# Optimization experiments

Hardware: AMD Instinct MI355X
Metric: run time of the kernel (lower is better)

Reference implementation:

```python
import jax, jax.numpy as jnp
import numpy as np

N = 50000
E = 400000
C = 64
H = 6  # heads, hardcoded in the module
NEG_SLOPE = 0.2
EPS = 1e-8


def setup_inputs() -> dict:
    key = jax.random.key(0)
    ks = jax.random.split(key, 10)
    x = jax.random.normal(ks[0], (N, C), dtype=jnp.float32)
    ei = jax.random.randint(ks[1], (2, E), 0, N)
    loop = jnp.arange(N)
    # forward() first calls add_remaining_self_loops -> GCN consumes edges + self loops
    src = jnp.concatenate([ei[0], loop])
    dst = jnp.concatenate([ei[1], loop])
    # gen_subs: subindex = self loops (i->i) plus reversed edges (t->i) for edge (i,t)
    sub_src = jnp.concatenate([loop, ei[1]])
    sub_dst = jnp.concatenate([loop, ei[0]])

    def glorot(k, shape):
        stdv = np.sqrt(6.0 / (shape[-2] + shape[-1]))
        return jax.random.uniform(k, shape, jnp.float32, -stdv, stdv)

    W_gcn = glorot(ks[2], (C, C))           # gnn_intra_cluster (GCNConv)
    b_gcn = jnp.zeros((C,), jnp.float32)
    weight = glorot(ks[3], (C, H * C))      # self.weight
    attention = glorot(ks[4], (1, H, 2 * C))  # self.attention
    W1 = glorot(ks[5], (C, C))              # simiConv.lin1 (no bias)
    W2 = glorot(ks[6], (C, 1))              # simiConv.lin2
    b2 = jnp.zeros((1,), jnp.float32)
    return {"x": x, "W_gcn": W_gcn, "b_gcn": b_gcn, "weight": weight,
            "attention": attention, "W1": W1, "W2": W2, "b2": b2,
            "src": src, "dst": dst, "sub_src": sub_src, "sub_dst": sub_dst}


def _gcn(x, W, b, src, dst, n):
    # PyG GCNConv's gcn_norm appends its own self loops on top of the ones
    # already added by forward()'s add_remaining_self_loops.
    loop = jnp.arange(n)
    s = jnp.concatenate([src, loop])
    d = jnp.concatenate([dst, loop])
    deg = jax.ops.segment_sum(jnp.ones_like(s, dtype=x.dtype), d, num_segments=n)
    dinv = jax.lax.rsqrt(jnp.maximum(deg, 1.0e-12))
    norm = dinv[s] * dinv[d]                      # [E']
    h = x @ W                                     # [N, C]
    out = jax.ops.segment_sum(h[s] * norm[:, None], d, num_segments=n)
    return out + b


def reference(x, W_gcn, b_gcn, weight, attention, W1, W2, b2,
              src, dst, sub_src, sub_dst):
    n = x.shape[0]
    # intra-cluster GCN
    xpj = _gcn(x, W_gcn, b_gcn, src, dst, n)      # [N, C]
    # multi-head attention pooling over subindex
    h = (xpj @ weight).reshape(n, H, C)           # [N, H, C]
    hi = h[sub_src]                               # [Es, H, C] (x_i in message)
    hmax = jax.ops.segment_max(hi, sub_dst, num_segments=n)  # [N, H, C]
    att_i = attention[:, :, :C]                   # [1, H, C]
    att_j = attention[:, :, C:]
    alpha = (hi * att_i).sum(-1) + (hmax[sub_dst] * att_j).sum(-1)  # [Es, H]
    alpha = jnp.where(alpha >= 0, alpha, NEG_SLOPE * alpha)
    # segment softmax over destination nodes (dropout p=0)
    amax = jax.ops.segment_max(alpha, sub_dst, num_segments=n)
    e = jnp.exp(alpha - amax[sub_dst])
    denom = jax.ops.segment_sum(e, sub_dst, num_segments=n)
    alpha = e / denom[sub_dst]
    xa = jax.ops.segment_sum(hi * alpha[:, :, None], sub_dst, num_segments=n)
    xm = xa.mean(axis=1)                          # [N, C]
    # simiConv score: message = x_cluster_i * cos(x_i, x_j), aggr='add'
    a = xm @ W1                                   # [N, C]
    bsc = xm @ W2 + b2                            # [N, 1]
    ai = a[sub_dst]
    aj = a[sub_src]
    cos = (ai * aj).sum(-1) / (jnp.maximum(jnp.linalg.norm(ai, axis=-1), EPS)
                               * jnp.maximum(jnp.linalg.norm(aj, axis=-1), EPS))
    score = jax.ops.segment_sum(bsc[sub_dst, 0] * cos, sub_dst, num_segments=n)
    fitness = jax.nn.sigmoid(score)               # [N]
    return fitness
```

## Files before the change

### kernel.cpp

```cpp
#include <hip/hip_runtime.h>
#include <math.h>

#define TPB 256
#define NEG_SLOPE 0.2f
#define COS_EPS 1e-8f
#define NH 6
#define GSTRIDE 68
#define DCACHE 12
#define SALS 8

__device__ inline float wave_sum64(float v) {
  #pragma unroll
  for (int off = 32; off > 0; off >>= 1) v += __shfl_down(v, off);
  return __shfl(v, 0);
}
__device__ inline float wave_max64(float v) {
  #pragma unroll
  for (int off = 32; off > 0; off >>= 1) v = fmaxf(v, __shfl_down(v, off));
  return __shfl(v, 0);
}
__device__ inline unsigned short f2bf(float f) {
  unsigned u = __float_as_uint(f);
  unsigned r = (u + 0x7fffu + ((u >> 16) & 1u)) >> 16;
  return (unsigned short)r;
}
__device__ inline float bf2f(unsigned short b) {
  return __uint_as_float(((unsigned)b) << 16);
}
__device__ inline unsigned packbf(float lo, float hi) {
  return (unsigned)f2bf(lo) | ((unsigned)f2bf(hi) << 16);
}
__device__ inline float bflo(unsigned u) { return __uint_as_float(u << 16); }
__device__ inline float bfhi(unsigned u) { return __uint_as_float(u & 0xffff0000u); }

#define GS_LOOP(i, total) \
  for (long i = (long)blockIdx.x * blockDim.x + threadIdx.x; i < (total); \
       i += (long)gridDim.x * blockDim.x)

__global__ void k_cnt(const int* __restrict__ dst, const int* __restrict__ sdst,
                      int* __restrict__ gcnt, int* __restrict__ scnt,
                      long en, long sen) {
  long mx = en > sen ? en : sen;
  GS_LOOP(e, mx) {
    if (e < en)  atomicAdd(&gcnt[dst[e]], 1);
    if (e < sen) atomicAdd(&scnt[sdst[e]], 1);
  }
}

__global__ __launch_bounds__(1024)
void k_scanA(const int* __restrict__ gcnt, const int* __restrict__ scnt,
             int* __restrict__ bsum, float* __restrict__ dinv, int n, int nb) {
  const int b = blockIdx.x;
  const bool isS = b >= nb;
  const int tb = isS ? b - nb : b;
  const int* cnt = isS ? scnt : gcnt;
  const int t = threadIdx.x;
  const int i0 = tb * 2048 + 2 * t;
  int v0 = (i0 < n) ? cnt[i0] : 0;
  int v1 = (i0 + 1 < n) ? cnt[i0 + 1] : 0;
  if (!isS) {
    if (i0 < n)     dinv[i0]     = rsqrtf((float)v0 + 1.0f);
    if (i0 + 1 < n) dinv[i0 + 1] = rsqrtf((float)v1 + 1.0f);
  }
  __shared__ int red[16];
  int x = v0 + v1;
  #pragma unroll
  for (int o = 32; o > 0; o >>= 1) x += __shfl_down(x, o);
  const int lane = t & 63, wv = t >> 6;
  if (lane == 0) red[wv] = x;
  __syncthreads();
  if (t < 64) {
    int w = (t < 16) ? red[t] : 0;
    #pragma unroll
    for (int o = 32; o > 0; o >>= 1) w += __shfl_down(w, o);
    if (t == 0) bsum[b] = w;
  }
}

__global__ void k_scanB(int* __restrict__ bsum, int nb) {
  const int lane = threadIdx.x;
  if (nb <= 32) {
    int half = lane >> 5, idx = lane & 31;
    int base = half * nb;
    int v = (idx < nb) ? bsum[base + idx] : 0;
    int orig = v;
    #pragma unroll
    for (int d2 = 1; d2 < 32; d2 <<= 1) {
      int y = __shfl_up(v, d2, 32);
      if (idx >= d2) v += y;
    }
    if (idx < nb) bsum[base + idx] = v - orig;
  } else if (lane == 0) {
    int run = 0;
    for (int i = 0; i < nb; ++i) { int v = bsum[i]; bsum[i] = run; run += v; }
    run = 0;
    for (int i = 0; i < nb; ++i) { int v = bsum[nb + i]; bsum[nb + i] = run; run += v; }
  }
}

__global__ __launch_bounds__(1024)
void k_scanC(const int* __restrict__ gcnt, int* __restrict__ goff, int* __restrict__ gcur,
             const int* __restrict__ scnt, int* __restrict__ soff, int* __restrict__ scur,
             const int* __restrict__ bsum, int n, int nb) {
  const int b = blockIdx.x;
  const bool isS = b >= nb;
  const int tb = isS ? b - nb : b;
  const int* cnt = isS ? scnt : gcnt;
  int* off = isS ? soff : goff;
  int* cur = isS ? scur : gcur;
  const int t = threadIdx.x;
  const int i0 = tb * 2048 + 2 * t;
  int v0 = (i0 < n) ? cnt[i0] : 0;
  int v1 = (i0 + 1 < n) ? cnt[i0 + 1] : 0;
  int s2 = v0 + v1;
  const int lane = t & 63, wv = t >> 6;
  int x = s2;
  #pragma unroll
  for (int d2 = 1; d2 < 64; d2 <<= 1) {
    int y = __shfl_up(x, d2);
    if (lane >= d2) x += y;
  }
  __shared__ int wsum[16];
  if (lane == 63) wsum[wv] = x;
  __syncthreads();
  if (t < 64) {
    int w = (t < 16) ? wsum[t] : 0;
    #pragma unroll
    for (int d2 = 1; d2 < 16; d2 <<= 1) {
      int y = __shfl_up(w, d2);
      if ((int)t >= d2) w += y;
    }
    if (t < 16) wsum[t] = w;
  }
  __syncthreads();
  int ex = x - s2 + (wv ? wsum[wv - 1] : 0) + bsum[b];
  if (i0 < n)     { cur[i0] = ex;          off[i0 + 1] = ex + v0; }
  if (i0 + 1 < n) { cur[i0 + 1] = ex + v0; off[i0 + 2] = ex + v0 + v1; }
  if (i0 == 0) off[0] = 0;
}

__global__ void k_scatter(const int* __restrict__ src, const int* __restrict__ dst,
                          const int* __restrict__ ssrc, const int* __restrict__ sdst,
                          int* __restrict__ gcur, int* __restrict__ gcsr,
                          int* __restrict__ scur, int* __restrict__ scsr,
                          long en, long sen) {
  long mx = en > sen ? en : sen;
  GS_LOOP(e, mx) {
    if (e < en)  { int d = dst[e];  int p = atomicAdd(&gcur[d], 1); gcsr[p] = src[e]; }
    if (e < sen) { int d = sdst[e]; int p = atomicAdd(&scur[d], 1); scsr[p] = ssrc[e]; }
  }
}

template <int MODE>
__global__ __launch_bounds__(256)
void k_gemm64v3(const float* __restrict__ A, const float* __restrict__ W,
                float* __restrict__ out32, unsigned short* __restrict__ out16,
                const float* __restrict__ W2, const float* __restrict__ b2,
                float* __restrict__ bsc, int n, int Mtot) {
  __shared__ float At[64 * GSTRIDE];
  __shared__ float Wl[64 * GSTRIDE];
  const int t  = threadIdx.x;
  const int tx = t & 15;
  const int ty = t >> 4;
  const int col0 = blockIdx.y * 64;
  const long row0 = (long)blockIdx.x * 64;

  #pragma unroll
  for (int i = 0; i < 4; ++i) {
    int k = ty + 16 * i;
    float4 wv = *(const float4*)&W[(long)k * Mtot + col0 + 4 * tx];
    *(float4*)&Wl[k * GSTRIDE + 4 * tx] = wv;
  }
  #pragma unroll
  for (int i = 0; i < 4; ++i) {
    int r = ty + 16 * i;
    long gr = row0 + r; if (gr >= n) gr = n - 1;
    float4 av = *(const float4*)&A[gr * 64 + 4 * tx];
    At[(4 * tx + 0) * GSTRIDE + r] = av.x;
    At[(4 * tx + 1) * GSTRIDE + r] = av.y;
    At[(4 * tx + 2) * GSTRIDE + r] = av.z;
    At[(4 * tx + 3) * GSTRIDE + r] = av.w;
  }
  __syncthreads();

  const int c0 = 4 * tx;
  const int r0 = 4 * ty;
  float acc[4][4] = {};
  #pragma unroll
  for (int k = 0; k < 64; ++k) {
    float4 av = *(const float4*)&At[k * GSTRIDE + r0];
    float4 wv = *(const float4*)&Wl[k * GSTRIDE + c0];
    acc[0][0] = fmaf(av.x, wv.x, acc[0][0]); acc[0][1] = fmaf(av.x, wv.y, acc[0][1]);
    acc[0][2] = fmaf(av.x, wv.z, acc[0][2]); acc[0][3] = fmaf(av.x, wv.w, acc[0][3]);
    acc[1][0] = fmaf(av.y, wv.x, acc[1][0]); acc[1][1] = fmaf(av.y, wv.y, acc[1][1]);
    acc[1][2] = fmaf(av.y, wv.z, acc[1][2]); acc[1][3] = fmaf(av.y, wv.w, acc[1][3]);
    acc[2][0] = fmaf(av.z, wv.x, acc[2][0]); acc[2][1] = fmaf(av.z, wv.y, acc[2][1]);
    acc[2][2] = fmaf(av.z, wv.z, acc[2][2]); acc[2][3] = fmaf(av.z, wv.w, acc[2][3]);
    acc[3][0] = fmaf(av.w, wv.x, acc[3][0]); acc[3][1] = fmaf(av.w, wv.y, acc[3][1]);
    acc[3][2] = fmaf(av.w, wv.z, acc[3][2]); acc[3][3] = fmaf(av.w, wv.w, acc[3][3]);
  }

  if constexpr (MODE == 0) {
    #pragma unroll
    for (int i = 0; i < 4; ++i) {
      long gr = row0 + r0 + i;
      if (gr < n)
        *(float4*)&out32[gr * Mtot + col0 + c0] =
          make_float4(acc[i][0], acc[i][1], acc[i][2], acc[i][3]);
    }
  }
  if constexpr (MODE == 2) {
    float p[4], q[4];
    #pragma unroll
    for (int i = 0; i < 4; ++i) {
      q[i] = acc[i][0]*acc[i][0] + acc[i][1]*acc[i][1] +
             acc[i][2]*acc[i][2] + acc[i][3]*acc[i][3];
      p[i] = At[(c0+0) * GSTRIDE + r0 + i] * W2[c0+0] +
             At[(c0+1) * GSTRIDE + r0 + i] * W2[c0+1] +
             At[(c0+2) * GSTRIDE + r0 + i] * W2[c0+2] +
             At[(c0+3) * GSTRIDE + r0 + i] * W2[c0+3];
    }
    #pragma unroll
    for (int m = 1; m < 16; m <<= 1) {
      #pragma unroll
      for (int i = 0; i < 4; ++i) { p[i] += __shfl_xor(p[i], m); q[i] += __shfl_xor(q[i], m); }
    }
    float bb = b2[0];
    #pragma unroll
    for (int i = 0; i < 4; ++i) {
      long gr = row0 + r0 + i;
      if (gr < n) {
        float rn = 1.0f / fmaxf(sqrtf(q[i]), COS_EPS);
        ushort4 v;
        v.x = f2bf(acc[i][0] * rn); v.y = f2bf(acc[i][1] * rn);
        v.z = f2bf(acc[i][2] * rn); v.w = f2bf(acc[i][3] * rn);
        *(ushort4*)&out16[gr * 64 + c0] = v;
        if (tx == 0) bsc[gr] = p[i] + bb;
      }
    }
  }
}

__global__ __launch_bounds__(256)
void k_gemm_h2(const float* __restrict__ A, const float* __restrict__ W,
               unsigned* __restrict__ h2p, const float* __restrict__ att,
               float* __restrict__ sal, int n) {
  __shared__ float At[64 * GSTRIDE];
  __shared__ float Wl[64 * GSTRIDE];
  const int t  = threadIdx.x;
  const int tx = t & 15;
  const int ty = t >> 4;
  const long row0 = (long)blockIdx.x * 64;
  const int c0 = 4 * tx;
  const int r0 = 4 * ty;

  #pragma unroll
  for (int i = 0; i < 4; ++i) {
    int r = ty + 16 * i;
    long gr = row0 + r; if (gr >= n) gr = n - 1;
    float4 av = *(const float4*)&A[gr * 64 + 4 * tx];
    At[(4 * tx + 0) * GSTRIDE + r] = av.x;
    At[(4 * tx + 1) * GSTRIDE + r] = av.y;
    At[(4 * tx + 2) * GSTRIDE + r] = av.z;
    At[(4 * tx + 3) * GSTRIDE + r] = av.w;
  }
  float4 wr[4];
  #pragma unroll
  for (int i = 0; i < 4; ++i)
    wr[i] = *(const float4*)&W[(long)(ty + 16 * i) * 384 + 4 * tx];

  float4 acc[6][4];
  #pragma unroll
  for (int h = 0; h < 6; ++h)
    #pragma unroll
    for (int i = 0; i < 4; ++i) acc[h][i] = make_float4(0.f, 0.f, 0.f, 0.f);

  #pragma unroll
  for (int head = 0; head < 6; ++head) {
    #pragma unroll
    for (int i = 0; i < 4; ++i)
      *(float4*)&Wl[(ty + 16 * i) * GSTRIDE + 4 * tx] = wr[i];
    __syncthreads();
    if (head < 5) {
      #pragma unroll
      for (int i = 0; i < 4; ++i)
        wr[i] = *(const float4*)&W[(long)(ty + 16 * i) * 384 + (head + 1) * 64 + 4 * tx];
    }
    #pragma unroll 16
    for (int k = 0; k < 64; ++k) {
      float4 av = *(const float4*)&At[k * GSTRIDE + r0];
      float4 wv = *(const float4*)&Wl[k * GSTRIDE + c0];
      acc[head][0].x = fmaf(av.x, wv.x, acc[head][0].x);
      acc[head][0].y = fmaf(av.x, wv.y, acc[head][0].y);
      acc[head][0].z = fmaf(av.x, wv.z, acc[head][0].z);
      acc[head][0].w = fmaf(av.x, wv.w, acc[head][0].w);
      acc[head][1].x = fmaf(av.y, wv.x, acc[head][1].x);
      acc[head][1].y = fmaf(av.y, wv.y, acc[head][1].y);
      acc[head][1].z = fmaf(av.y, wv.z, acc[head][1].z);
      acc[head][1].w = fmaf(av.y, wv.w, acc[head][1].w);
      acc[head][2].x = fmaf(av.z, wv.x, acc[head][2].x);
      acc[head][2].y = fmaf(av.z, wv.y, acc[head][2].y);
      acc[head][2].z = fmaf(av.z, wv.z, acc[head][2].z);
      acc[head][2].w = fmaf(av.z, wv.w, acc[head][2].w);
      acc[head][3].x = fmaf(av.w, wv.x, acc[head][3].x);
      acc[head][3].y = fmaf(av.w, wv.y, acc[head][3].y);
      acc[head][3].z = fmaf(av.w, wv.z, acc[head][3].z);
      acc[head][3].w = fmaf(av.w, wv.w, acc[head][3].w);
    }
    __syncthreads();
  }

  #pragma unroll
  for (int i = 0; i < 4; ++i) {
    long gr = row0 + r0 + i;
    if (gr < n) {
      uint4 u0, u1, u2;
      u0.x = packbf(acc[0][i].x, acc[1][i].x);
      u0.y = packbf(acc[2][i].x, acc[3][i].x);
      u0.z = packbf(acc[4][i].x, acc[5][i].x);
      u0.w = packbf(acc[0][i].y, acc[1][i].y);
      u1.x = packbf(acc[2][i].y, acc[3][i].y);
      u1.y = packbf(acc[4][i].y, acc[5][i].y);
      u1.z = packbf(acc[0][i].z, acc[1][i].z);
      u1.w = packbf(acc[2][i].z, acc[3][i].z);
      u2.x = packbf(acc[4][i].z, acc[5][i].z);
      u2.y = packbf(acc[0][i].w, acc[1][i].w);
      u2.z = packbf(acc[2][i].w, acc[3][i].w);
      u2.w = packbf(acc[4][i].w, acc[5][i].w);
      unsigned* dst = &h2p[gr * 192 + c0 * 3];
      *(uint4*)(dst + 0) = u0;
      *(uint4*)(dst + 4) = u1;
      *(uint4*)(dst + 8) = u2;
    }
  }
  #pragma unroll
  for (int head = 0; head < 6; ++head) {
    float a0 = att[head * 128 + c0 + 0], a1 = att[head * 128 + c0 + 1];
    float a2 = att[head * 128 + c0 + 2], a3 = att[head * 128 + c0 + 3];
    float p[4];
    #pragma unroll
    for (int i = 0; i < 4; ++i)
      p[i] = acc[head][i].x * a0 + acc[head][i].y * a1 +
             acc[head][i].z * a2 + acc[head][i].w * a3;
    #pragma unroll
    for (int m = 1; m < 16; m <<= 1) {
      #pragma unroll
      for (int i = 0; i < 4; ++i) p[i] += __shfl_xor(p[i], m);
    }
    if (tx == 0) {
      #pragma unroll
      for (int i = 0; i < 4; ++i) {
        long gr = row0 + r0 + i;
        if (gr < n) sal[gr * SALS + head] = p[i];
      }
    }
  }
}

__global__ __launch_bounds__(256)
void k_gcn_csr(const int* __restrict__ goff, const int* __restrict__ gcsr,
               const float* __restrict__ h, const float* __restrict__ dinv,
               const float* __restrict__ bg, float* __restrict__ xpj, int n) {
  const int lane = threadIdx.x & 63;
  const int d = blockIdx.x * 4 + (threadIdx.x >> 6);
  if (d >= n) return;
  const int o0 = goff[d], o1 = goff[d + 1];
  float acc = 0.f;
  int j = o0;
  for (; j + 1 < o1; j += 2) {
    int s0 = gcsr[j], s1 = gcsr[j + 1];
    float f0 = h[(long)s0 * 64 + lane], f1 = h[(long)s1 * 64 + lane];
    acc = fmaf(f0, dinv[s0], acc);
    acc = fmaf(f1, dinv[s1], acc);
  }
  if (j < o1) { int s0 = gcsr[j]; acc = fmaf(h[(long)s0 * 64 + lane], dinv[s0], acc); }
  float di = dinv[d];
  xpj[(long)d * 64 + lane] = bg[lane] + di * acc + h[(long)d * 64 + lane] * di * di;
}

__global__ __launch_bounds__(256)
void k_mega(const int* __restrict__ soff, const int* __restrict__ scsr,
            const unsigned* __restrict__ h2p, const float* __restrict__ sal,
            const float* __restrict__ att, float* __restrict__ xm, int n) {
  const int lane = threadIdx.x & 63;
  const int d = blockIdx.x * 4 + (threadIdx.x >> 6);
  if (d >= n) return;
  const int o0 = soff[d], o1 = soff[d + 1];
  const int deg = o1 - o0;

  unsigned ck0[DCACHE], ck1[DCACHE], ck2[DCACHE];
  float hm[NH];
  #pragma unroll
  for (int h = 0; h < NH; ++h) hm[h] = -INFINITY;
  #pragma unroll
  for (int idx = 0; idx < DCACHE; ++idx) {
    unsigned u0 = 0, u1 = 0, u2 = 0;
    if (idx < deg) {
      long s = scsr[o0 + idx];
      const unsigned* rp = &h2p[s * 192 + lane * 3];
      u0 = rp[0]; u1 = rp[1]; u2 = rp[2];
      hm[0] = fmaxf(hm[0], bflo(u0)); hm[1] = fmaxf(hm[1], bfhi(u0));
      hm[2] = fmaxf(hm[2], bflo(u1)); hm[3] = fmaxf(hm[3], bfhi(u1));
      hm[4] = fmaxf(hm[4], bflo(u2)); hm[5] = fmaxf(hm[5], bfhi(u2));
    }
    ck0[idx] = u0; ck1[idx] = u1; ck2[idx] = u2;
  }
  for (int j = o0 + DCACHE; j < o1; ++j) {
    long s = scsr[j];
    const unsigned* rp = &h2p[s * 192 + lane * 3];
    unsigned u0 = rp[0], u1 = rp[1], u2 = rp[2];
    hm[0] = fmaxf(hm[0], bflo(u0)); hm[1] = fmaxf(hm[1], bfhi(u0));
    hm[2] = fmaxf(hm[2], bflo(u1)); hm[3] = fmaxf(hm[3], bfhi(u1));
    hm[4] = fmaxf(hm[4], bflo(u2)); hm[5] = fmaxf(hm[5], bfhi(u2));
  }

  float dal[NH];
  #pragma unroll
  for (int h = 0; h < NH; ++h)
    dal[h] = wave_sum64(hm[h] * att[h * 128 + 64 + lane]);

  float acc[NH], den[NH];
  #pragma unroll
  for (int h = 0; h < NH; ++h) acc[h] = 0.f;

  if (deg <= 64) {
    const bool act = lane < deg;
    int sE = 0;
    float4 sA = make_float4(0, 0, 0, 0), sB = sA;
    if (act) {
      sE = scsr[o0 + lane];
      const float4* sp = (const float4*)&sal[(long)sE * SALS];
      sA = sp[0]; sB = sp[1];
    }
    float svv[NH] = {sA.x, sA.y, sA.z, sA.w, sB.x, sB.y};
    float e6[NH];
    #pragma unroll
    for (int h = 0; h < NH; ++h) {
      float al = svv[h] + dal[h];
      al = (al >= 0.f) ? al : NEG_SLOPE * al;
      float a = act ? al : -INFINITY;
      float mx = wave_max64(a);
      e6[h] = act ? expf(a - mx) : 0.f;
      den[h] = wave_sum64(e6[h]);
    }
    #pragma unroll
    for (int idx = 0; idx < DCACHE; ++idx) {
      if (idx < deg) {
        float w0 = __shfl(e6[0], idx), w1 = __shfl(e6[1], idx);
        float w2 = __shfl(e6[2], idx), w3 = __shfl(e6[3], idx);
        float w4 = __shfl(e6[4], idx), w5 = __shfl(e6[5], idx);
        acc[0] = fmaf(bflo(ck0[idx]), w0, acc[0]);
        acc[1] = fmaf(bfhi(ck0[idx]), w1, acc[1]);
        acc[2] = fmaf(bflo(ck1[idx]), w2, acc[2]);
        acc[3] = fmaf(bfhi(ck1[idx]), w3, acc[3]);
        acc[4] = fmaf(bflo(ck2[idx]), w4, acc[4]);
        acc[5] = fmaf(bfhi(ck2[idx]), w5, acc[5]);
      }
    }
    for (int j = o0 + DCACHE; j < o1; ++j) {
      int ii = j - o0;
      long s = scsr[j];
      const unsigned* rp = &h2p[s * 192 + lane * 3];
      unsigned u0 = rp[0], u1 = rp[1], u2 = rp[2];
      float w0 = __shfl(e6[0], ii), w1 = __shfl(e6[1], ii);
      float w2 = __shfl(e6[2], ii), w3 = __shfl(e6[3], ii);
      float w4 = __shfl(e6[4], ii), w5 = __shfl(e6[5], ii);
      acc[0] = fmaf(bflo(u0), w0, acc[0]);
      acc[1] = fmaf(bfhi(u0), w1, acc[1]);
      acc[2] = fmaf(bflo(u1), w2, acc[2]);
      acc[3] = fmaf(bfhi(u1), w3, acc[3]);
      acc[4] = fmaf(bflo(u2), w4, acc[4]);
      acc[5] = fmaf(bfhi(u2), w5, acc[5]);
    }
  } else {
    float mx[NH];
    #pragma unroll
    for (int h = 0; h < NH; ++h) { mx[h] = -INFINITY; den[h] = 0.f; }
    for (int base = o0; base < o1; base += 64) {
      int j = base + lane;
      float a6[NH];
      if (j < o1) {
        long s = scsr[j];
        const float4* sp = (const float4*)&sal[s * SALS];
        float4 sA = sp[0], sB = sp[1];
        float svv[NH] = {sA.x, sA.y, sA.z, sA.w, sB.x, sB.y};
        #pragma unroll
        for (int h = 0; h < NH; ++h) {
          float al = svv[h] + dal[h];
          a6[h] = (al >= 0.f) ? al : NEG_SLOPE * al;
        }
      } else {
        #pragma unroll
        for (int h = 0; h < NH; ++h) a6[h] = -INFINITY;
      }
      #pragma unroll
      for (int h = 0; h < NH; ++h) mx[h] = fmaxf(mx[h], wave_max64(a6[h]));
    }
    for (int base = o0; base < o1; base += 64) {
      int cs = o1 - base; if (cs > 64) cs = 64;
      int j = base + lane;
      float e6[NH]; int s = 0;
      if (j < o1) {
        s = scsr[j];
        const float4* sp = (const float4*)&sal[(long)s * SALS];
        float4 sA = sp[0], sB = sp[1];
        float svv[NH] = {sA.x, sA.y, sA.z, sA.w, sB.x, sB.y};
        #pragma unroll
        for (int h = 0; h < NH; ++h) {
          float al = svv[h] + dal[h];
          al = (al >= 0.f) ? al : NEG_SLOPE * al;
          e6[h] = expf(al - mx[h]);
        }
      } else {
        #pragma unroll
        for (int h = 0; h < NH; ++h) e6[h] = 0.f;
      }
      #pragma unroll
      for (int h = 0; h < NH; ++h) den[h] += wave_sum64(e6[h]);
      for (int jj = 0; jj < cs; ++jj) {
        int sj = __shfl(s, jj);
        const unsigned* rp = &h2p[(long)sj * 192 + lane * 3];
        unsigned u0 = rp[0], u1 = rp[1], u2 = rp[2];
        float w0 = __shfl(e6[0], jj), w1 = __shfl(e6[1], jj);
        float w2 = __shfl(e6[2], jj), w3 = __shfl(e6[3], jj);
        float w4 = __shfl(e6[4], jj), w5 = __shfl(e6[5], jj);
        acc[0] = fmaf(bflo(u0), w0, acc[0]);
        acc[1] = fmaf(bfhi(u0), w1, acc[1]);
        acc[2] = fmaf(bflo(u1), w2, acc[2]);
        acc[3] = fmaf(bfhi(u1), w3, acc[3]);
        acc[4] = fmaf(bflo(u2), w4, acc[4]);
        acc[5] = fmaf(bfhi(u2), w5, acc[5]);
      }
    }
  }

  float o = 0.f;
  #pragma unroll
  for (int h = 0; h < NH; ++h) o += acc[h] / den[h];
  xm[(long)d * 64 + lane] = o * (1.0f / NH);
}

__global__ __launch_bounds__(256)
void k_cosout(const int* __restrict__ soff, const int* __restrict__ scsr,
              const unsigned short* __restrict__ an, const float* __restrict__ bsc,
              float* __restrict__ out, int n) {
  const int lane = threadIdx.x & 63;
  const int d = blockIdx.x * 4 + (threadIdx.x >> 6);
  if (d >= n) return;
  const int o0 = soff[d], o1 = soff[d + 1];
  float ad = bf2f(an[(long)d * 64 + lane]);
  float cl = 0.f;
  int j = o0;
  for (; j + 1 < o1; j += 2) {
    int s0 = scsr[j], s1 = scsr[j + 1];
    float f0 = bf2f(an[(long)s0 * 64 + lane]);
    float f1 = bf2f(an[(long)s1 * 64 + lane]);
    cl = fmaf(ad, f0, cl);
    cl = fmaf(ad, f1, cl);
  }
  if (j < o1) { int s0 = scsr[j]; cl = fmaf(ad, bf2f(an[(long)s0 * 64 + lane]), cl); }
  float cs = wave_sum64(cl);
  if (lane == 0) out[d] = 1.0f / (1.0f + expf(-bsc[d] * cs));
}

static inline unsigned gsblocks(long total) {
  long b = (total + TPB - 1) / TPB;
  if (b > 131072) b = 131072;
  return (unsigned)b;
}

extern "C" void kernel_launch(void* const* d_in, const int* in_sizes, int n_in,
                              void* d_out, int out_size, void* d_ws, size_t ws_size,
                              hipStream_t stream) {
  const float* x   = (const float*)d_in[0];
  const float* Wg  = (const float*)d_in[1];
  const float* bg  = (const float*)d_in[2];
  const float* Wt  = (const float*)d_in[3];
  const float* att = (const float*)d_in[4];
  const float* W1  = (const float*)d_in[5];
  const float* W2  = (const float*)d_in[6];
  const float* b2  = (const float*)d_in[7];
  const int* src   = (const int*)d_in[8];
  const int* dst   = (const int*)d_in[9];
  const int* ssrc  = (const int*)d_in[10];
  const int* sdst  = (const int*)d_in[11];

  const long n   = in_sizes[0] / 64;
  const long en  = in_sizes[8];
  const long sen = in_sizes[10];
  const int  nb  = (int)((n + 2047) / 2048);

  char* base = (char*)d_ws;
  size_t off = 0;
  auto alloc = [&](size_t bytes) -> void* {
    void* p = base + off;
    off += (bytes + 255) & ~(size_t)255;
    return p;
  };
  int*   gcnt = (int*)alloc(n * 4);
  int*   scnt = (int*)alloc(n * 4);
  int*   goff = (int*)alloc((n + 1) * 4);
  int*   soff = (int*)alloc((n + 1) * 4);
  int*   gcur = (int*)alloc(n * 4);
  int*   scur = (int*)alloc(n * 4);
  int*   gcsr = (int*)alloc(en * 4);
  int*   scsr = (int*)alloc(sen * 4);
  int*   bsum = (int*)alloc(2 * (size_t)nb * 4);
  float* dinv = (float*)alloc(n * 4);
  float* h    = (float*)alloc(n * 64 * 4);
  float* xpj  = (float*)alloc(n * 64 * 4);
  unsigned* h2p = (unsigned*)alloc(n * 192 * 4);
  float* sal  = (float*)alloc(n * SALS * 4);
  float* bsc  = (float*)alloc(n * 4);
  float* xm   = h;
  unsigned short* anorm = (unsigned short*)xpj;
  float* out  = (float*)d_out;

  const unsigned rowblk  = (unsigned)((n + 63) / 64);
  const unsigned nodeblk = (unsigned)((n + 3) / 4);

  hipMemsetAsync(gcnt, 0, (size_t)((char*)scnt - (char*)gcnt) + n * 4, stream);
  k_cnt<<<gsblocks(en), TPB, 0, stream>>>(dst, sdst, gcnt, scnt, en, sen);
  k_scanA<<<2 * nb, 1024, 0, stream>>>(gcnt, scnt, bsum, dinv, (int)n, nb);
  k_scanB<<<1, 64, 0, stream>>>(bsum, nb);
  k_scanC<<<2 * nb, 1024, 0, stream>>>(gcnt, goff, gcur, scnt, soff, scur,
                                       bsum, (int)n, nb);
  k_scatter<<<gsblocks(en), TPB, 0, stream>>>(src, dst, ssrc, sdst,
                                              gcur, gcsr, scur, scsr, en, sen);

  { dim3 g(rowblk, 1);
    k_gemm64v3<0><<<g, 256, 0, stream>>>(x, Wg, h, nullptr,
                                         nullptr, nullptr, nullptr, (int)n, 64); }

  k_gcn_csr<<<nodeblk, 256, 0, stream>>>(goff, gcsr, h, dinv, bg, xpj, (int)n);

  k_gemm_h2<<<rowblk, 256, 0, stream>>>(xpj, Wt, h2p, att, sal, (int)n);

  k_mega<<<nodeblk, 256, 0, stream>>>(soff, scsr, h2p, sal, att, xm, (int)n);

  { dim3 g(rowblk, 1);
    k_gemm64v3<2><<<g, 256, 0, stream>>>(xm, W1, nullptr, anorm,
                                         W2, b2, bsc, (int)n, 64); }

  k_cosout<<<nodeblk, 256, 0, stream>>>(soff, scsr, anorm, bsc, out, (int)n);
}
```

Baseline: 375.6 us.

## Reorder GCN to aggregate bf16 prescaled x before the weight GEMM

The GCN is reordered so that neighbour aggregation runs on x prescaled by dinv and packed to bf16, and the 64x64 GEMM with bias then runs on the aggregated result. This cuts the gather bytes per edge in half and removes the per-neighbour dinv load. The count and scatter kernels now process two edges per thread with int2 loads, and the cosine gather reads packed bf16 pairs with two edges per wave. The trade-off is extra precision loss from rounding x to bf16 and one extra prep kernel.

```diff
diff --git a/kernel.cpp b/kernel.cpp
--- a/kernel.cpp
+++ b/kernel.cpp
@@ -40,10 +40,17 @@
 __global__ void k_cnt(const int* __restrict__ dst, const int* __restrict__ sdst,
                       int* __restrict__ gcnt, int* __restrict__ scnt,
                       long en, long sen) {
-  long mx = en > sen ? en : sen;
-  GS_LOOP(e, mx) {
-    if (e < en)  atomicAdd(&gcnt[dst[e]], 1);
-    if (e < sen) atomicAdd(&scnt[sdst[e]], 1);
+  long mx = ((en > sen ? en : sen) + 1) >> 1;
+  GS_LOOP(e2, mx) {
+    long e = 2 * e2;
+    if (e + 1 < en) {
+      int2 v = *(const int2*)&dst[e];
+      atomicAdd(&gcnt[v.x], 1); atomicAdd(&gcnt[v.y], 1);
+    } else if (e < en) atomicAdd(&gcnt[dst[e]], 1);
+    if (e + 1 < sen) {
+      int2 v = *(const int2*)&sdst[e];
+      atomicAdd(&scnt[v.x], 1); atomicAdd(&scnt[v.y], 1);
+    } else if (e < sen) atomicAdd(&scnt[sdst[e]], 1);
   }
 }
 
@@ -144,10 +151,66 @@
                           int* __restrict__ gcur, int* __restrict__ gcsr,
                           int* __restrict__ scur, int* __restrict__ scsr,
                           long en, long sen) {
-  long mx = en > sen ? en : sen;
-  GS_LOOP(e, mx) {
-    if (e < en)  { int d = dst[e];  int p = atomicAdd(&gcur[d], 1); gcsr[p] = src[e]; }
-    if (e < sen) { int d = sdst[e]; int p = atomicAdd(&scur[d], 1); scsr[p] = ssrc[e]; }
+  long mx = ((en > sen ? en : sen) + 1) >> 1;
+  GS_LOOP(e2, mx) {
+    long e = 2 * e2;
+    if (e + 1 < en) {
+      int2 s = *(const int2*)&src[e];
+      int2 d = *(const int2*)&dst[e];
+      int p0 = atomicAdd(&gcur[d.x], 1); gcsr[p0] = s.x;
+      int p1 = atomicAdd(&gcur[d.y], 1); gcsr[p1] = s.y;
+    } else if (e < en) {
+      int p = atomicAdd(&gcur[dst[e]], 1); gcsr[p] = src[e];
+    }
+    if (e + 1 < sen) {
+      int2 s = *(const int2*)&ssrc[e];
+      int2 d = *(const int2*)&sdst[e];
+      int p0 = atomicAdd(&scur[d.x], 1); scsr[p0] = s.x;
+      int p1 = atomicAdd(&scur[d.y], 1); scsr[p1] = s.y;
+    } else if (e < sen) {
+      int p = atomicAdd(&scur[sdst[e]], 1); scsr[p] = ssrc[e];
+    }
+  }
+}
+
+__global__ void k_xprep(const float* __restrict__ x, const float* __restrict__ dinv,
+                        unsigned* __restrict__ xb, long n) {
+  GS_LOOP(idx, n * 32) {
+    long i = idx >> 5; int p = (int)(idx & 31);
+    float di = dinv[i];
+    float2 xv = *(const float2*)&x[i * 64 + 2 * p];
+    xb[idx] = packbf(xv.x * di, xv.y * di);
+  }
+}
+
+__global__ __launch_bounds__(256)
+void k_gcn2(const int* __restrict__ goff, const int* __restrict__ gcsr,
+            const unsigned* __restrict__ xb, const float* __restrict__ x,
+            const float* __restrict__ dinv, float* __restrict__ xagg, int n) {
+  const int lane = threadIdx.x & 63;
+  const int p = lane & 31;
+  const int hf = lane >> 5;
+  const int d = blockIdx.x * 4 + (threadIdx.x >> 6);
+  if (d >= n) return;
+  const int o0 = goff[d], o1 = goff[d + 1];
+  float ax = 0.f, ay = 0.f;
+  for (int j = o0; j < o1; j += 2) {
+    int jj = j + hf;
+    if (jj < o1) {
+      long s = gcsr[jj];
+      unsigned u = xb[s * 32 + p];
+      ax += bflo(u); ay += bfhi(u);
+    }
+  }
+  ax += __shfl_xor(ax, 32);
+  ay += __shfl_xor(ay, 32);
+  if (hf == 0) {
+    float di = dinv[d];
+    float2 xd = *(const float2*)&x[(long)d * 64 + 2 * p];
+    float2 r;
+    r.x = di * ax + xd.x * di * di;
+    r.y = di * ay + xd.y * di * di;
+    *(float2*)&xagg[(long)d * 64 + 2 * p] = r;
   }
 }
 
@@ -155,6 +218,7 @@
 __global__ __launch_bounds__(256)
 void k_gemm64v3(const float* __restrict__ A, const float* __restrict__ W,
                 float* __restrict__ out32, unsigned short* __restrict__ out16,
+                const float* __restrict__ bias,
                 const float* __restrict__ W2, const float* __restrict__ b2,
                 float* __restrict__ bsc, int n, int Mtot) {
   __shared__ float At[64 * GSTRIDE];
@@ -201,12 +265,15 @@
   }
 
   if constexpr (MODE == 0) {
+    float4 bv = make_float4(0.f, 0.f, 0.f, 0.f);
+    if (bias) bv = *(const float4*)&bias[col0 + c0];
     #pragma unroll
     for (int i = 0; i < 4; ++i) {
       long gr = row0 + r0 + i;
       if (gr < n)
         *(float4*)&out32[gr * Mtot + col0 + c0] =
-          make_float4(acc[i][0], acc[i][1], acc[i][2], acc[i][3]);
+          make_float4(acc[i][0] + bv.x, acc[i][1] + bv.y,
+                      acc[i][2] + bv.z, acc[i][3] + bv.w);
     }
   }
   if constexpr (MODE == 2) {
@@ -327,10 +394,10 @@
       u2.y = packbf(acc[0][i].w, acc[1][i].w);
       u2.z = packbf(acc[2][i].w, acc[3][i].w);
       u2.w = packbf(acc[4][i].w, acc[5][i].w);
-      unsigned* dst = &h2p[gr * 192 + c0 * 3];
-      *(uint4*)(dst + 0) = u0;
-      *(uint4*)(dst + 4) = u1;
-      *(uint4*)(dst + 8) = u2;
+      unsigned* dstp = &h2p[gr * 192 + c0 * 3];
+      *(uint4*)(dstp + 0) = u0;
+      *(uint4*)(dstp + 4) = u1;
+      *(uint4*)(dstp + 8) = u2;
     }
   }
   #pragma unroll
@@ -355,27 +422,6 @@
       }
     }
   }
-}
-
-__global__ __launch_bounds__(256)
-void k_gcn_csr(const int* __restrict__ goff, const int* __restrict__ gcsr,
-               const float* __restrict__ h, const float* __restrict__ dinv,
-               const float* __restrict__ bg, float* __restrict__ xpj, int n) {
-  const int lane = threadIdx.x & 63;
-  const int d = blockIdx.x * 4 + (threadIdx.x >> 6);
-  if (d >= n) return;
-  const int o0 = goff[d], o1 = goff[d + 1];
-  float acc = 0.f;
-  int j = o0;
-  for (; j + 1 < o1; j += 2) {
-    int s0 = gcsr[j], s1 = gcsr[j + 1];
-    float f0 = h[(long)s0 * 64 + lane], f1 = h[(long)s1 * 64 + lane];
-    acc = fmaf(f0, dinv[s0], acc);
-    acc = fmaf(f1, dinv[s1], acc);
-  }
-  if (j < o1) { int s0 = gcsr[j]; acc = fmaf(h[(long)s0 * 64 + lane], dinv[s0], acc); }
-  float di = dinv[d];
-  xpj[(long)d * 64 + lane] = bg[lane] + di * acc + h[(long)d * 64 + lane] * di * di;
 }
 
 __global__ __launch_bounds__(256)
@@ -542,23 +588,25 @@
 
 __global__ __launch_bounds__(256)
 void k_cosout(const int* __restrict__ soff, const int* __restrict__ scsr,
-              const unsigned short* __restrict__ an, const float* __restrict__ bsc,
+              const unsigned* __restrict__ an32, const float* __restrict__ bsc,
               float* __restrict__ out, int n) {
   const int lane = threadIdx.x & 63;
+  const int p = lane & 31;
+  const int hf = lane >> 5;
   const int d = blockIdx.x * 4 + (threadIdx.x >> 6);
   if (d >= n) return;
   const int o0 = soff[d], o1 = soff[d + 1];
-  float ad = bf2f(an[(long)d * 64 + lane]);
+  unsigned ud = an32[(long)d * 32 + p];
+  float adx = bflo(ud), ady = bfhi(ud);
   float cl = 0.f;
-  int j = o0;
-  for (; j + 1 < o1; j += 2) {
-    int s0 = scsr[j], s1 = scsr[j + 1];
-    float f0 = bf2f(an[(long)s0 * 64 + lane]);
-    float f1 = bf2f(an[(long)s1 * 64 + lane]);
-    cl = fmaf(ad, f0, cl);
-    cl = fmaf(ad, f1, cl);
-  }
-  if (j < o1) { int s0 = scsr[j]; cl = fmaf(ad, bf2f(an[(long)s0 * 64 + lane]), cl); }
+  for (int j = o0; j < o1; j += 2) {
+    int jj = j + hf;
+    if (jj < o1) {
+      long s = scsr[jj];
+      unsigned u = an32[s * 32 + p];
+      cl += adx * bflo(u) + ady * bfhi(u);
+    }
+  }
   float cs = wave_sum64(cl);
   if (lane == 0) out[d] = 1.0f / (1.0f + expf(-bsc[d] * cs));
 }
@@ -607,11 +655,13 @@
   int*   scsr = (int*)alloc(sen * 4);
   int*   bsum = (int*)alloc(2 * (size_t)nb * 4);
   float* dinv = (float*)alloc(n * 4);
+  unsigned* xb = (unsigned*)alloc(n * 32 * 4);
   float* h    = (float*)alloc(n * 64 * 4);
   float* xpj  = (float*)alloc(n * 64 * 4);
   unsigned* h2p = (unsigned*)alloc(n * 192 * 4);
   float* sal  = (float*)alloc(n * SALS * 4);
   float* bsc  = (float*)alloc(n * 4);
+  float* xagg = h;
   float* xm   = h;
   unsigned short* anorm = (unsigned short*)xpj;
   float* out  = (float*)d_out;
@@ -620,27 +670,30 @@
   const unsigned nodeblk = (unsigned)((n + 3) / 4);
 
   hipMemsetAsync(gcnt, 0, (size_t)((char*)scnt - (char*)gcnt) + n * 4, stream);
-  k_cnt<<<gsblocks(en), TPB, 0, stream>>>(dst, sdst, gcnt, scnt, en, sen);
+  k_cnt<<<gsblocks((en + 1) / 2), TPB, 0, stream>>>(dst, sdst, gcnt, scnt, en, sen);
   k_scanA<<<2 * nb, 1024, 0, stream>>>(gcnt, scnt, bsum, dinv, (int)n, nb);
   k_scanB<<<1, 64, 0, stream>>>(bsum, nb);
   k_scanC<<<2 * nb, 1024, 0, stream>>>(gcnt, goff, gcur, scnt, soff, scur,
                                        bsum, (int)n, nb);
-  k_scatter<<<gsblocks(en), TPB, 0, stream>>>(src, dst, ssrc, sdst,
+  k_scatter<<<gsblocks((en + 1) / 2), TPB, 0, stream>>>(src, dst, ssrc, sdst,
                                               gcur, gcsr, scur, scsr, en, sen);
 
+  k_xprep<<<gsblocks(n * 32), TPB, 0, stream>>>(x, dinv, xb, n);
+
+  k_gcn2<<<nodeblk, 256, 0, stream>>>(goff, gcsr, xb, x, dinv, xagg, (int)n);
+
   { dim3 g(rowblk, 1);
-    k_gemm64v3<0><<<g, 256, 0, stream>>>(x, Wg, h, nullptr,
+    k_gemm64v3<0><<<g, 256, 0, stream>>>(xagg, Wg, xpj, nullptr, bg,
                                          nullptr, nullptr, nullptr, (int)n, 64); }
 
-  k_gcn_csr<<<nodeblk, 256, 0, stream>>>(goff, gcsr, h, dinv, bg, xpj, (int)n);
-
   k_gemm_h2<<<rowblk, 256, 0, stream>>>(xpj, Wt, h2p, att, sal, (int)n);
 
   k_mega<<<nodeblk, 256, 0, stream>>>(soff, scsr, h2p, sal, att, xm, (int)n);
 
   { dim3 g(rowblk, 1);
-    k_gemm64v3<2><<<g, 256, 0, stream>>>(xm, W1, nullptr, anorm,
+    k_gemm64v3<2><<<g, 256, 0, stream>>>(xm, W1, nullptr, anorm, nullptr,
                                          W2, b2, bsc, (int)n, 64); }
 
-  k_cosout<<<nodeblk, 256, 0, stream>>>(soff, scsr, anorm, bsc, out, (int)n);
-}
+  k_cosout<<<nodeblk, 256, 0, stream>>>(soff, scsr, (const unsigned*)anorm,
+                                        bsc, out, (int)n);
+}
```

Measured after the change: 427.7 us. 1.14x slower.
